# Kernel optimization log

Hardware: AMD Instinct MI355X
Metric: run time of the kernel (lower is better)

Reference implementation:

```python
import jax, jax.numpy as jnp
import numpy as np

N_EXPERTS = 64
TOP_K = 2
LOAD_BALANCE_COEF = 0.01
D_MODEL = 4096
N_TOKENS = 16384


def setup_inputs() -> dict:
    key = jax.random.key(0)
    kx, kw = jax.random.split(key)
    x = jax.random.normal(kx, (N_TOKENS, D_MODEL), dtype=jnp.float32)
    # nn.init.normal_(gate.weight, std=0.01); shape (n_experts, d_model)
    gate_w = 0.01 * jax.random.normal(kw, (N_EXPERTS, D_MODEL), dtype=jnp.float32)
    return {"x": x, "gate_w": gate_w}


def reference(x, gate_w):
    # logits: (N, n_experts)
    logits = jnp.einsum('nd,ed->ne', x, gate_w)
    router_probs = jax.nn.softmax(logits, axis=-1)
    top_k_weights, top_k_indices = jax.lax.top_k(router_probs, TOP_K)
    routing_weights = top_k_weights / jnp.sum(top_k_weights, axis=-1, keepdims=True)
    top1 = top_k_indices[:, 0]
    one_hot = jax.nn.one_hot(top1, N_EXPERTS, dtype=x.dtype)  # (N, n_experts)
    f_i = jnp.mean(one_hot, axis=0)          # fraction of tokens per expert (detached)
    p_i = jnp.mean(router_probs, axis=0)     # mean router prob per expert (diff.)
    load_balance_loss = LOAD_BALANCE_COEF * jnp.sum(jax.lax.stop_gradient(f_i) * p_i)
    return routing_weights, top_k_indices, load_balance_loss
```

## Files before the change

### kernel.cpp

```cpp
#include <hip/hip_runtime.h>
#include <math.h>

#define N_TOKENS 16384
#define D_MODEL  4096
#define N_EXP    64

#define TOKB  64
#define NWV   16
#define NSL   8
#define KSL   (D_MODEL / NSL)
#define CH    16
#define NCH   (KSL / CH)
#define PPAD  36
#define PFOFF (NWV * TOKB * PPAD)
#define NBLK  (N_TOKENS / TOKB)

__global__ void __launch_bounds__(256)
transpose_w(const float* __restrict__ w, float* __restrict__ wt) {
    __shared__ float t[64][65];
    const int k0 = blockIdx.x * 64;
    const int kc = (threadIdx.x & 15) * 4;
    const int e0 = threadIdx.x >> 4;
#pragma unroll
    for (int p = 0; p < 4; ++p) {
        int e = p * 16 + e0;
        float4 v = *(const float4*)(w + (size_t)e * D_MODEL + k0 + kc);
        t[kc + 0][e] = v.x; t[kc + 1][e] = v.y;
        t[kc + 2][e] = v.z; t[kc + 3][e] = v.w;
    }
    __syncthreads();
    const int kr = threadIdx.x >> 2;
    const int ec = (threadIdx.x & 3) * 16;
#pragma unroll
    for (int j = 0; j < 4; ++j) {
        float4 v = make_float4(t[kr][ec + j * 4 + 0], t[kr][ec + j * 4 + 1],
                               t[kr][ec + j * 4 + 2], t[kr][ec + j * 4 + 3]);
        *(float4*)(wt + (size_t)(k0 + kr) * N_EXP + ec + j * 4) = v;
    }
}

__global__ void __launch_bounds__(1024)
router_fused(const float* __restrict__ x, const float* __restrict__ wt,
             float* __restrict__ out, float* __restrict__ block_sums) {
    __shared__ float part[PFOFF + 2 * NWV * 64];

    const int tid  = threadIdx.x;
    const int wid  = tid >> 6;
    const int lane = tid & 63;
    const int tok0 = blockIdx.x * TOKB;

    const int wid_u = __builtin_amdgcn_readfirstlane(wid);
    const int h = wid_u & 1;
    const int s = wid_u >> 1;

    const float* xr = x + (size_t)(tok0 + lane) * D_MODEL + s * KSL;
    const float* wr = wt + (size_t)s * KSL * N_EXP + h * 32;

    float acc[32] = {};

    float4 xa0 = *(const float4*)(xr + 0);
    float4 xa1 = *(const float4*)(xr + 4);
    float4 xa2 = *(const float4*)(xr + 8);
    float4 xa3 = *(const float4*)(xr + 12);

#pragma unroll 1
    for (int g = 0; g < NCH; ++g) {
        float4 xb0, xb1, xb2, xb3;
        if (g + 1 < NCH) {
            const float* xn = xr + (g + 1) * CH;
            xb0 = *(const float4*)(xn + 0);
            xb1 = *(const float4*)(xn + 4);
            xb2 = *(const float4*)(xn + 8);
            xb3 = *(const float4*)(xn + 12);
        }
        const float xc[CH] = {xa0.x, xa0.y, xa0.z, xa0.w,
                              xa1.x, xa1.y, xa1.z, xa1.w,
                              xa2.x, xa2.y, xa2.z, xa2.w,
                              xa3.x, xa3.y, xa3.z, xa3.w};
        const float* wg = wr + (size_t)g * CH * N_EXP;
#pragma unroll
        for (int k = 0; k < CH; ++k) {
            const float* wk = wg + k * N_EXP;
            const float xk = xc[k];
#pragma unroll
            for (int e = 0; e < 32; ++e)
                acc[e] = fmaf(wk[e], xk, acc[e]);
        }
        xa0 = xb0; xa1 = xb1; xa2 = xb2; xa3 = xb3;
    }

    {
        float* tp = part + (size_t)(wid * TOKB + lane) * PPAD;
#pragma unroll
        for (int e0 = 0; e0 < 32; e0 += 4)
            *(float4*)(tp + e0) = make_float4(acc[e0], acc[e0 + 1],
                                              acc[e0 + 2], acc[e0 + 3]);
    }
    __syncthreads();

    float p_acc = 0.f, f_acc = 0.f;
    const int he = lane >> 5;
    const int ew = lane & 31;
#pragma unroll 1
    for (int it = 0; it < 4; ++it) {
        const int tl = wid * 4 + it;
        float logit = 0.f;
#pragma unroll
        for (int sl = 0; sl < NSL; ++sl)
            logit += part[(size_t)((2 * sl + he) * TOKB + tl) * PPAD + ew];

        float m = logit;
#pragma unroll
        for (int off = 32; off; off >>= 1)
            m = fmaxf(m, __shfl_xor(m, off, 64));
        unsigned long long b1 = __ballot(logit == m);
        int i1 = __ffsll(b1) - 1;

        float p = expf(logit - m);
        float denom = p;
#pragma unroll
        for (int off = 32; off; off >>= 1)
            denom += __shfl_xor(denom, off, 64);

        p_acc += p / denom;
        if (lane == i1) f_acc += 1.f;

        float lx = (lane == i1) ? -__builtin_inff() : logit;
        float m2 = lx;
#pragma unroll
        for (int off = 32; off; off >>= 1)
            m2 = fmaxf(m2, __shfl_xor(m2, off, 64));
        unsigned long long b2 = __ballot(lx == m2);
        int i2 = __ffsll(b2) - 1;

        if (lane == 0) {
            float p1 = 1.0f / denom;
            float p2 = expf(m2 - m) / denom;
            float s12 = p1 + p2;
            int token = tok0 + tl;
            ((float2*)out)[token] = make_float2(p1 / s12, p2 / s12);
            ((float2*)(out + 2 * N_TOKENS))[token] =
                make_float2((float)i1, (float)i2);
        }
    }

    float* pf = part + PFOFF;
    pf[wid * 64 + lane]        = p_acc;
    pf[1024 + wid * 64 + lane] = f_acc;
    __syncthreads();
    if (tid < N_EXP) {
        float ps = 0.f, fs = 0.f;
#pragma unroll
        for (int hh = 0; hh < NWV; ++hh) {
            ps += pf[hh * 64 + tid];
            fs += pf[1024 + hh * 64 + tid];
        }
        block_sums[(size_t)blockIdx.x * 128 + tid]      = ps;
        block_sums[(size_t)blockIdx.x * 128 + 64 + tid] = fs;
    }
}

__global__ void __launch_bounds__(256)
router_final(const float* __restrict__ block_sums, float* __restrict__ out) {
    __shared__ float sp[4][N_EXP];
    __shared__ float sf[4][N_EXP];

    int tid  = threadIdx.x;
    int wv   = tid >> 6;
    int lane = tid & 63;

    float ps = 0.f, fs = 0.f;
#pragma unroll 8
    for (int b = wv * (NBLK / 4); b < (wv + 1) * (NBLK / 4); ++b) {
        ps += block_sums[(size_t)b * 128 + lane];
        fs += block_sums[(size_t)b * 128 + 64 + lane];
    }
    sp[wv][lane] = ps;
    sf[wv][lane] = fs;
    __syncthreads();

    if (tid < N_EXP) {
        float pt = sp[0][tid] + sp[1][tid] + sp[2][tid] + sp[3][tid];
        float ft = sf[0][tid] + sf[1][tid] + sf[2][tid] + sf[3][tid];
        float v = pt * ft;
#pragma unroll
        for (int off = 1; off < 64; off <<= 1)
            v += __shfl_xor(v, off, 64);
        if (tid == 0)
            out[4 * N_TOKENS] = 0.01f * v / ((float)N_TOKENS * (float)N_TOKENS);
    }
}

extern "C" void kernel_launch(void* const* d_in, const int* in_sizes, int n_in,
                              void* d_out, int out_size, void* d_ws, size_t ws_size,
                              hipStream_t stream) {
    (void)in_sizes; (void)n_in; (void)out_size; (void)ws_size;
    const float* x = (const float*)d_in[0];
    const float* w = (const float*)d_in[1];
    float* out = (float*)d_out;

    float* wT = (float*)d_ws;
    float* block_sums = wT + (size_t)D_MODEL * N_EXP;

    transpose_w<<<D_MODEL / 64, 256, 0, stream>>>(w, wT);
    router_fused<<<NBLK, 1024, 0, stream>>>(x, wT, out, block_sums);
    router_final<<<1, 256, 0, stream>>>(block_sums, out);
}
```

Before: 419.2 us.

## Stage x tiles cooperatively through double-buffered LDS and tree-reduce slice partials

Each wave pair now loads its 64-token by 16-k slice of x cooperatively with coalesced float4 loads. The slice is written transposed into a double-buffered LDS tile, so both expert-half waves read x from shared memory instead of each lane streaming its own token row twice from global memory. The cross-slice reduction of partial logits becomes a staged LDS tree reduction that produces a single logit table, which the softmax and top-k stage then reads directly. The cost is a block-wide barrier for every k-chunk in a 1024-thread block, plus extra LDS traffic and barriers during the reduction.

```diff
diff --git a/kernel.cpp b/kernel.cpp
--- a/kernel.cpp
+++ b/kernel.cpp
@@ -5,15 +5,15 @@
 #define D_MODEL  4096
 #define N_EXP    64
 
-#define TOKB  64
-#define NWV   16
-#define NSL   8
-#define KSL   (D_MODEL / NSL)
-#define CH    16
-#define NCH   (KSL / CH)
-#define PPAD  36
-#define PFOFF (NWV * TOKB * PPAD)
-#define NBLK  (N_TOKENS / TOKB)
+#define TOKB 64
+#define NWV  16
+#define NSL  8
+#define KSL  (D_MODEL / NSL)
+#define BK   16
+#define NCH  (KSL / BK)
+#define XLD  66
+#define SLSZ (2 * BK * XLD)
+#define NBLK (N_TOKENS / TOKB)
 
 __global__ void __launch_bounds__(256)
 transpose_w(const float* __restrict__ w, float* __restrict__ wt) {
@@ -42,7 +42,7 @@
 __global__ void __launch_bounds__(1024)
 router_fused(const float* __restrict__ x, const float* __restrict__ wt,
              float* __restrict__ out, float* __restrict__ block_sums) {
-    __shared__ float part[PFOFF + 2 * NWV * 64];
+    __shared__ float smem[NSL * SLSZ];
 
     const int tid  = threadIdx.x;
     const int wid  = tid >> 6;
@@ -53,61 +53,105 @@
     const int h = wid_u & 1;
     const int s = wid_u >> 1;
 
-    const float* xr = x + (size_t)(tok0 + lane) * D_MODEL + s * KSL;
+    float* xsl = smem + s * SLSZ;
+
+    const int p  = tid & 127;
+    const int t0 = p >> 2;
+    const int kc = (p & 3) * 4;
+
     const float* wr = wt + (size_t)s * KSL * N_EXP + h * 32;
+    const float* xgb = x + (size_t)(tok0 + t0) * D_MODEL + s * KSL + kc;
 
     float acc[32] = {};
 
-    float4 xa0 = *(const float4*)(xr + 0);
-    float4 xa1 = *(const float4*)(xr + 4);
-    float4 xa2 = *(const float4*)(xr + 8);
-    float4 xa3 = *(const float4*)(xr + 12);
-
+    {
+        float4 v0 = *(const float4*)(xgb);
+        float4 v1 = *(const float4*)(xgb + (size_t)32 * D_MODEL);
+#pragma unroll
+        for (int i = 0; i < 4; ++i) {
+            xsl[(kc + i) * XLD + t0]      = ((const float*)&v0)[i];
+            xsl[(kc + i) * XLD + t0 + 32] = ((const float*)&v1)[i];
+        }
+    }
+    __syncthreads();
+
+    int cur = 0;
 #pragma unroll 1
     for (int g = 0; g < NCH; ++g) {
-        float4 xb0, xb1, xb2, xb3;
+        float4 v0, v1;
         if (g + 1 < NCH) {
-            const float* xn = xr + (g + 1) * CH;
-            xb0 = *(const float4*)(xn + 0);
-            xb1 = *(const float4*)(xn + 4);
-            xb2 = *(const float4*)(xn + 8);
-            xb3 = *(const float4*)(xn + 12);
-        }
-        const float xc[CH] = {xa0.x, xa0.y, xa0.z, xa0.w,
-                              xa1.x, xa1.y, xa1.z, xa1.w,
-                              xa2.x, xa2.y, xa2.z, xa2.w,
-                              xa3.x, xa3.y, xa3.z, xa3.w};
-        const float* wg = wr + (size_t)g * CH * N_EXP;
-#pragma unroll
-        for (int k = 0; k < CH; ++k) {
-            const float* wk = wg + k * N_EXP;
-            const float xk = xc[k];
+            const float* xg = xgb + (g + 1) * BK;
+            v0 = *(const float4*)(xg);
+            v1 = *(const float4*)(xg + (size_t)32 * D_MODEL);
+        }
+
+        const float* xb = xsl + cur * (BK * XLD) + lane;
+        const float* wg = wr + (size_t)g * BK * N_EXP;
+#pragma unroll
+        for (int k = 0; k < BK; ++k) {
+            const float xk = xb[k * XLD];
+            const float* wk = wg + (size_t)k * N_EXP;
 #pragma unroll
             for (int e = 0; e < 32; ++e)
                 acc[e] = fmaf(wk[e], xk, acc[e]);
         }
-        xa0 = xb0; xa1 = xb1; xa2 = xb2; xa3 = xb3;
-    }
-
-    {
-        float* tp = part + (size_t)(wid * TOKB + lane) * PPAD;
-#pragma unroll
-        for (int e0 = 0; e0 < 32; e0 += 4)
-            *(float4*)(tp + e0) = make_float4(acc[e0], acc[e0 + 1],
-                                              acc[e0 + 2], acc[e0 + 3]);
+
+        if (g + 1 < NCH) {
+            float* bn = xsl + (cur ^ 1) * (BK * XLD);
+#pragma unroll
+            for (int i = 0; i < 4; ++i) {
+                bn[(kc + i) * XLD + t0]      = ((const float*)&v0)[i];
+                bn[(kc + i) * XLD + t0 + 32] = ((const float*)&v1)[i];
+            }
+        }
+        __syncthreads();
+        cur ^= 1;
+    }
+
+    if (s >= 4) {
+        float* tp = smem + (((s - 4) * 2 + h) * 64 + lane) * 33;
+#pragma unroll
+        for (int e = 0; e < 32; ++e) tp[e] = acc[e];
+    }
+    __syncthreads();
+    if (s < 4) {
+        const float* tp = smem + ((s * 2 + h) * 64 + lane) * 33;
+#pragma unroll
+        for (int e = 0; e < 32; ++e) acc[e] += tp[e];
+    }
+    __syncthreads();
+    if (s == 2 || s == 3) {
+        float* tp = smem + (((s - 2) * 2 + h) * 64 + lane) * 33;
+#pragma unroll
+        for (int e = 0; e < 32; ++e) tp[e] = acc[e];
+    }
+    __syncthreads();
+    if (s < 2) {
+        const float* tp = smem + ((s * 2 + h) * 64 + lane) * 33;
+#pragma unroll
+        for (int e = 0; e < 32; ++e) acc[e] += tp[e];
+    }
+    __syncthreads();
+    if (s == 1) {
+        float* tp = smem + (h * 64 + lane) * 33;
+#pragma unroll
+        for (int e = 0; e < 32; ++e) tp[e] = acc[e];
+    }
+    __syncthreads();
+    float* flog = smem + 8448;
+    if (s == 0) {
+        const float* tp = smem + (h * 64 + lane) * 33;
+#pragma unroll
+        for (int e = 0; e < 32; ++e)
+            flog[lane * 65 + h * 32 + e] = acc[e] + tp[e];
     }
     __syncthreads();
 
     float p_acc = 0.f, f_acc = 0.f;
-    const int he = lane >> 5;
-    const int ew = lane & 31;
 #pragma unroll 1
     for (int it = 0; it < 4; ++it) {
         const int tl = wid * 4 + it;
-        float logit = 0.f;
-#pragma unroll
-        for (int sl = 0; sl < NSL; ++sl)
-            logit += part[(size_t)((2 * sl + he) * TOKB + tl) * PPAD + ew];
+        float logit = flog[tl * 65 + lane];
 
         float m = logit;
 #pragma unroll
@@ -116,13 +160,13 @@
         unsigned long long b1 = __ballot(logit == m);
         int i1 = __ffsll(b1) - 1;
 
-        float p = expf(logit - m);
-        float denom = p;
+        float pr = expf(logit - m);
+        float denom = pr;
 #pragma unroll
         for (int off = 32; off; off >>= 1)
             denom += __shfl_xor(denom, off, 64);
 
-        p_acc += p / denom;
+        p_acc += pr / denom;
         if (lane == i1) f_acc += 1.f;
 
         float lx = (lane == i1) ? -__builtin_inff() : logit;
@@ -144,7 +188,7 @@
         }
     }
 
-    float* pf = part + PFOFF;
+    float* pf = smem + 12608;
     pf[wid * 64 + lane]        = p_acc;
     pf[1024 + wid * 64 + lane] = f_acc;
     __syncthreads();
```

Result: slower. 719.6 us (+71.7%).
